# Kernel tuning notes

Measured on AMD Instinct MI355X. Metric: run time of the kernel, lower is better.

## Reference

```python
import jax, jax.numpy as jnp
import numpy as np

DIN = 256
N_RATIOS = 3          # cfg.ANCHOR_RATIOS = [0.5, 1, 2]
NC_SCORE = N_RATIOS * 2   # 6
NC_BBOX = N_RATIOS * 4    # 12
LEVEL_SHAPES = [(150, 250), (75, 125), (38, 63), (19, 32), (10, 16)]


def setup_inputs() -> dict:
    key = jax.random.key(0)
    ks = jax.random.split(key, 12)
    inp = {}
    for i, (h, w) in enumerate(LEVEL_SHAPES):
        inp[f"rpn_feat_p{i+2}"] = jax.random.normal(ks[i], (4, DIN, h, w), dtype=jnp.float32)
    inp["im_info"] = jnp.ones((4, 3), dtype=jnp.float32)
    s = 0.01
    inp["W_conv"] = jax.random.normal(ks[5], (512, DIN, 3, 3), dtype=jnp.float32) * s
    inp["b_conv"] = jnp.zeros((512,), dtype=jnp.float32)
    inp["W_cls"] = jax.random.normal(ks[6], (NC_SCORE, 512), dtype=jnp.float32) * s
    inp["b_cls"] = jnp.zeros((NC_SCORE,), dtype=jnp.float32)
    inp["W_box"] = jax.random.normal(ks[7], (NC_BBOX, 512), dtype=jnp.float32) * s
    inp["b_box"] = jnp.zeros((NC_BBOX,), dtype=jnp.float32)
    return inp


def _conv3x3(x, W, b):
    y = jax.lax.conv_general_dilated(
        x, W, window_strides=(1, 1), padding="SAME",
        dimension_numbers=("NCHW", "OIHW", "NCHW"))
    return y + b[None, :, None, None]


def _level_head(feat, W_conv, b_conv, W_cls, b_cls, W_box, b_box):
    B = feat.shape[0]
    conv1 = jax.nn.relu(_conv3x3(feat, W_conv, b_conv))            # [B,512,H,W]
    score = jnp.einsum("bchw,oc->bohw", conv1, W_cls) + b_cls[None, :, None, None]  # [B,6,H,W]
    bbox = jnp.einsum("bchw,oc->bohw", conv1, W_box) + b_box[None, :, None, None]   # [B,12,H,W]
    _, C, H, W = score.shape
    # reshape(x, 2): view(B, 2, C*H/2, W), softmax over dim 1, reshape back
    prob = jax.nn.softmax(score.reshape(B, 2, (C * H) // 2, W), axis=1).reshape(B, C, H, W)
    score_f = score.transpose(0, 2, 3, 1).reshape(B, -1, 2)
    prob_f = prob.transpose(0, 2, 3, 1).reshape(B, -1, 2)
    bbox_f = bbox.transpose(0, 2, 3, 1).reshape(B, -1, 4)
    return score_f, prob_f, bbox_f


def reference(rpn_feat_p2, rpn_feat_p3, rpn_feat_p4, rpn_feat_p5, rpn_feat_p6,
              im_info, W_conv, b_conv, W_cls, b_cls, W_box, b_box):
    feats = [rpn_feat_p2, rpn_feat_p3, rpn_feat_p4, rpn_feat_p5, rpn_feat_p6]
    scores, probs, boxes = [], [], []
    for f in feats:  # fixed 5 FPN levels
        s, p, b = _level_head(f, W_conv, b_conv, W_cls, b_cls, W_box, b_box)
        scores.append(s); probs.append(p); boxes.append(b)
    rpn_cls_score_alls = jnp.concatenate(scores, axis=1)            # [B, N, 2]
    rpn_cls_prob_alls = jnp.concatenate(probs, axis=1)              # [B, N, 2]
    rpn_bbox_pred_alls = jnp.concatenate(boxes, axis=1)             # [B, N, 4]
    return rpn_cls_score_alls, rpn_cls_prob_alls, rpn_bbox_pred_alls
```

## Files before the change

kernel.cpp:

```cpp
#include <hip/hip_runtime.h>
#include <stdint.h>


typedef __bf16 bf16x8 __attribute__((ext_vector_type(8)));
typedef float  f32x4  __attribute__((ext_vector_type(4)));

#define WS_WR2_OFF   0
#define WS_WH2_OFF   2359296
#define WS_SB_OFF    2392064
#define WS_FP_OFF    17100800
#define WS_TOTAL     123197440

__device__ __forceinline__ unsigned short f2bf(float f) {
    unsigned u = __builtin_bit_cast(unsigned, f);
    unsigned r = (u + 0x7FFF + ((u >> 16) & 1)) >> 16;
    return (unsigned short)r;
}

__device__ __forceinline__ void gl_lds16(const void* g, void* l) {
    __builtin_amdgcn_global_load_lds(
        (const __attribute__((address_space(1))) unsigned int*)g,
        (__attribute__((address_space(3))) unsigned int*)l, 16, 0, 0);
}

__global__ __launch_bounds__(256) void prep_weights(
    const float* __restrict__ Wc, const float* __restrict__ Wcls,
    const float* __restrict__ Wbox,
    unsigned short* __restrict__ wr2, unsigned short* __restrict__ wh2)
{
    int idx = blockIdx.x * 256 + threadIdx.x;
    if (idx < 1179648) {
        int o = idx / 2304;
        int k = idx - o * 2304;
        int r = k >> 8, c = k & 255;
        wr2[idx] = f2bf(Wc[o * 2304 + c * 9 + r]);
    } else {
        int i2 = idx - 1179648;
        if (i2 < 16384) {
            int j = i2 >> 9, o = i2 & 511;
            float v = (j < 6) ? Wcls[j * 512 + o]
                    : (j < 18) ? Wbox[(j - 6) * 512 + o] : 0.0f;
            wh2[j * 512 + o] = f2bf(v);
        }
    }
}

__global__ __launch_bounds__(256) void zero_rings(unsigned short* __restrict__ fpad)
{
    int idx = blockIdx.x * 256 + threadIdx.x;
    int b = idx / 50432;
    int rem = idx - b * 50432;
    int Wp, H, W; long lb;
    if (rem < 25728)      {               Wp=252; H=150; W=250; lb=32768    + (long)b*9805824; }
    else if (rem < 38656) { rem -= 25728; Wp=127; H=75;  W=125; lb=39288832 + (long)b*2503424; }
    else if (rem < 45248) { rem -= 38656; Wp=65;  H=38;  W=63;  lb=49335296 + (long)b*665600;  }
    else if (rem < 48640) { rem -= 45248; Wp=34;  H=19;  W=32;  lb=52030464 + (long)b*182784;  }
    else                  { rem -= 48640; Wp=18;  H=10;  W=16;  lb=52794368 + (long)b*55296;   }
    int c = rem >> 5, slot = rem & 31;
    int h, w;
    if (c < Wp)          { h = 0;     w = c; }
    else if (c < 2 * Wp) { h = H + 1; w = c - Wp; }
    else {
        int c2 = c - 2 * Wp;
        h = 1 + (c2 >> 1);
        w = (c2 & 1) ? (W + 1) : 0;
    }
    uint4 z = {0u, 0u, 0u, 0u};
    *(uint4*)(fpad + lb + (long)(h * Wp + w) * 256 + slot * 8) = z;
}

__global__ __launch_bounds__(256) void prep_feats(
    const float* __restrict__ f0, const float* __restrict__ f1,
    const float* __restrict__ f2, const float* __restrict__ f3,
    const float* __restrict__ f4, unsigned short* __restrict__ fpad)
{
    __shared__ unsigned short lds[64 * 258];
    int bi = blockIdx.x;
    int b = bi / 817;
    int r = bi - b * 817;
    const float* fsrc; int H, W, Wp, h, wb; long lb;
    if (r < 600)      { fsrc=f0; H=150; W=250; Wp=252; h=r>>2; wb=r&3; lb=32768    + (long)b*9805824; }
    else if (r < 750) { int rr=r-600; fsrc=f1; H=75; W=125; Wp=127; h=rr>>1; wb=rr&1; lb=39288832 + (long)b*2503424; }
    else if (r < 788) { fsrc=f2; H=38; W=63; Wp=65; h=r-750; wb=0; lb=49335296 + (long)b*665600; }
    else if (r < 807) { fsrc=f3; H=19; W=32; Wp=34; h=r-788; wb=0; lb=52030464 + (long)b*182784; }
    else              { fsrc=f4; H=10; W=16; Wp=18; h=r-807; wb=0; lb=52794368 + (long)b*55296; }
    const int t = threadIdx.x;
    const long cstr = (long)H * W;
    const int w = t & 63;
    const int wg = wb * 64 + w;
    const bool wv = (wg < W);
    const float* src = fsrc + (((long)b * 256) * H + h) * W + wg;
    unsigned* ldsw = (unsigned*)lds;
    #pragma unroll 4
    for (int it = 0; it < 32; ++it) {
        int c0 = (t >> 6) * 2 + it * 8;
        float v0 = wv ? src[(long)c0 * cstr] : 0.0f;
        float v1 = wv ? src[(long)(c0 + 1) * cstr] : 0.0f;
        unsigned pk = (unsigned)f2bf(v0) | ((unsigned)f2bf(v1) << 16);
        ldsw[w * 129 + (c0 >> 1)] = pk;
    }
    __syncthreads();
    #pragma unroll
    for (int k = 0; k < 8; ++k) {
        int g  = k * 256 + t;
        int px = g >> 5;
        int pg = wb * 64 + px;
        if (pg >= W) continue;
        int d0 = px * 129 + (g & 31) * 4;
        uint4 v;
        v.x = ldsw[d0]; v.y = ldsw[d0 + 1]; v.z = ldsw[d0 + 2]; v.w = ldsw[d0 + 3];
        unsigned short* dst = fpad + lb + (long)((h + 1) * Wp + (pg + 1)) * 256 + (g & 31) * 8;
        *(uint4*)dst = v;
    }
}

__global__ __launch_bounds__(256) void conv_main(
    const unsigned short* __restrict__ fpad,
    const unsigned short* __restrict__ wr2,
    const unsigned short* __restrict__ wh2,
    const float* __restrict__ b_conv,
    float* __restrict__ sbuf)
{
    __shared__ unsigned short smem[16384];
    const int tid = threadIdx.x;
    const int bid = blockIdx.x;
    const int tile = ((bid >> 5) << 3) + (bid & 7);
    const int chunk = (bid >> 3) & 3;
    if (tile >= 1596) return;
    int b = tile / 399;
    int tr = tile - b * 399;
    int Wp, lt; long lb;
    if (tr < 296)      { lt = tr;       Wp = 252; lb = 32768    + (long)b * 9805824; }
    else if (tr < 371) { lt = tr - 296; Wp = 127; lb = 39288832 + (long)b * 2503424; }
    else if (tr < 391) { lt = tr - 371; Wp = 65;  lb = 49335296 + (long)b * 665600;  }
    else if (tr < 397) { lt = tr - 391; Wp = 34;  lb = 52030464 + (long)b * 182784;  }
    else               { lt = tr - 397; Wp = 18;  lb = 52794368 + (long)b * 55296;   }

    const int arow  = tid >> 3;
    const int aslot = (tid & 7) ^ (arow & 7);
    const long apix = lb + (long)(Wp + lt * 128 + arow) * 256 + aslot * 8;
    const long bofs = (long)(chunk * 128 + arow) * 2304 + aslot * 8;

    const int wv = tid >> 6, lane = tid & 63;
    char* lA = (char*)smem + wv * 1024;
    char* lB = (char*)smem + 16384 + wv * 1024;
    const int mrow = (wv & 1) * 64, ncol = (wv >> 1) * 64;
    const int mr = lane & 15;
    const int kq = (lane >> 4) * 8;
    const int m7 = mr & 7;

    f32x4 acc[4][4];
    #pragma unroll
    for (int mt = 0; mt < 4; ++mt)
        #pragma unroll
        for (int nt = 0; nt < 4; ++nt) acc[mt][nt] = (f32x4){0.f, 0.f, 0.f, 0.f};

    for (int r = 0; r < 9; ++r) {
        const int doff = (r / 3 - 1) * Wp + (r % 3 - 1);
        const unsigned short* ga = fpad + apix + (long)doff * 256;
        const unsigned short* gb = wr2 + bofs + r * 256;
        for (int cb = 0; cb < 4; ++cb) {
            const unsigned short* ga2 = ga + cb * 64;
            const unsigned short* gb2 = gb + cb * 64;
            #pragma unroll
            for (int i = 0; i < 4; ++i) {
                gl_lds16(ga2 + i * 8192,  lA + i * 4096);
                gl_lds16(gb2 + i * 73728, lB + i * 4096);
            }
            __syncthreads();
            #pragma unroll
            for (int kk = 0; kk < 64; kk += 32) {
                const int sx = ((((kk >> 3) + (lane >> 4)) ^ m7) << 3);
                bf16x8 af[4], bfr[4];
                #pragma unroll
                for (int mt = 0; mt < 4; ++mt)
                    af[mt] = *(const bf16x8*)&smem[(mrow + mt * 16 + mr) * 64 + sx];
                #pragma unroll
                for (int nt = 0; nt < 4; ++nt)
                    bfr[nt] = *(const bf16x8*)&smem[8192 + (ncol + nt * 16 + mr) * 64 + sx];
                #pragma unroll
                for (int mt = 0; mt < 4; ++mt)
                    #pragma unroll
                    for (int nt = 0; nt < 4; ++nt)
                        acc[mt][nt] = __builtin_amdgcn_mfma_f32_16x16x32_bf16(
                            af[mt], bfr[nt], acc[mt][nt], 0, 0, 0);
            }
            __syncthreads();
        }
    }

    float bias[4];
    #pragma unroll
    for (int nt = 0; nt < 4; ++nt) bias[nt] = b_conv[chunk * 128 + ncol + nt * 16 + mr];
    #pragma unroll
    for (int mt = 0; mt < 4; ++mt)
        #pragma unroll
        for (int nt = 0; nt < 4; ++nt)
            #pragma unroll
            for (int q = 0; q < 4; ++q) {
                int row = mrow + mt * 16 + (lane >> 4) * 4 + q;
                int col = ncol + nt * 16 + mr;
                int sl  = (col >> 3) ^ (row & 7);
                smem[row * 128 + (sl << 3) + (col & 7)] =
                    f2bf(fmaxf(acc[mt][nt][q] + bias[nt], 0.0f));
            }
    __syncthreads();

    f32x4 acc2[2][2];
    #pragma unroll
    for (int mi = 0; mi < 2; ++mi)
        #pragma unroll
        for (int ni = 0; ni < 2; ++ni) acc2[mi][ni] = (f32x4){0.f, 0.f, 0.f, 0.f};
    #pragma unroll
    for (int ks = 0; ks < 4; ++ks) {
        const int sg = ks * 4 + (lane >> 4);
        bf16x8 ha[2], hb[2];
        #pragma unroll
        for (int mi = 0; mi < 2; ++mi) {
            int rowH = (wv * 2 + mi) * 16 + mr;
            ha[mi] = *(const bf16x8*)&smem[rowH * 128 + ((sg ^ m7) << 3)];
        }
        #pragma unroll
        for (int ni = 0; ni < 2; ++ni)
            hb[ni] = *(const bf16x8*)&wh2[(ni * 16 + mr) * 512 + chunk * 128 + ks * 32 + kq];
        #pragma unroll
        for (int mi = 0; mi < 2; ++mi)
            #pragma unroll
            for (int ni = 0; ni < 2; ++ni)
                acc2[mi][ni] = __builtin_amdgcn_mfma_f32_16x16x32_bf16(
                    ha[mi], hb[ni], acc2[mi][ni], 0, 0, 0);
    }
    const long slotbase = (long)tile * 128;
    #pragma unroll
    for (int ni = 0; ni < 2; ++ni) {
        int j = ni * 16 + mr;
        if (j < 18) {
            #pragma unroll
            for (int mi = 0; mi < 2; ++mi)
                #pragma unroll
                for (int q = 0; q < 4; ++q) {
                    int row = (wv * 2 + mi) * 16 + (lane >> 4) * 4 + q;
                    atomicAdd(&sbuf[(slotbase + row) * 18 + j], acc2[mi][ni][q]);
                }
        }
    }
}

__global__ __launch_bounds__(256) void finalize(
    const float* __restrict__ sbuf, const float* __restrict__ b_cls,
    const float* __restrict__ b_box, float* __restrict__ out)
{
    int idx = blockIdx.x * 256 + threadIdx.x;
    int tile = idx >> 7, m = idx & 127;
    int b = tile / 399;
    int tr = tile - b * 399;
    int hp, wp, H, W, noff;
    if (tr < 296)      { int f = 252 + (tr)       * 128 + m; hp = f / 252; wp = f - hp * 252; H = 150; W = 250; noff = 0; }
    else if (tr < 371) { int f = 127 + (tr - 296) * 128 + m; hp = f / 127; wp = f - hp * 127; H = 75;  W = 125; noff = 112500; }
    else if (tr < 391) { int f = 65  + (tr - 371) * 128 + m; hp = f / 65;  wp = f - hp * 65;  H = 38;  W = 63;  noff = 140625; }
    else if (tr < 397) { int f = 34  + (tr - 391) * 128 + m; hp = f / 34;  wp = f - hp * 34;  H = 19;  W = 32;  noff = 147807; }
    else               { int f = 18  + (tr - 397) * 128 + m; hp = f / 18;  wp = f - hp * 18;  H = 10;  W = 16;  noff = 149631; }
    if (hp < 1 || hp > H || wp < 1 || wp > W) return;

    const float* s = sbuf + (long)idx * 18;
    float sc[6], bb[12], pr[6];
    #pragma unroll
    for (int c = 0; c < 6; ++c) sc[c] = s[c] + b_cls[c];
    #pragma unroll
    for (int k = 0; k < 12; ++k) bb[k] = s[6 + k] + b_box[k];
    #pragma unroll
    for (int c = 0; c < 6; ++c) {
        int p = (c < 3) ? c + 3 : c - 3;
        pr[c] = 1.0f / (1.0f + expf(sc[p] - sc[c]));
    }
    int n = noff + ((hp - 1) * W + (wp - 1)) * 3;
    long o0 = ((long)b * 150111 + n) * 2;
    float* O0 = out + o0;
    float* O1 = out + 1200888 + o0;
    float* O2 = out + 2401776 + ((long)b * 150111 + n) * 4;
    #pragma unroll
    for (int c = 0; c < 6; ++c) { O0[c] = sc[c]; O1[c] = pr[c]; }
    #pragma unroll
    for (int k = 0; k < 12; ++k) O2[k] = bb[k];
}

extern "C" void kernel_launch(void* const* d_in, const int* in_sizes, int n_in,
                              void* d_out, int out_size, void* d_ws, size_t ws_size,
                              hipStream_t stream)
{
    const float* f0   = (const float*)d_in[0];
    const float* f1   = (const float*)d_in[1];
    const float* f2   = (const float*)d_in[2];
    const float* f3   = (const float*)d_in[3];
    const float* f4   = (const float*)d_in[4];
    const float* Wc   = (const float*)d_in[6];
    const float* bC   = (const float*)d_in[7];
    const float* Wcls = (const float*)d_in[8];
    const float* bcls = (const float*)d_in[9];
    const float* Wbox = (const float*)d_in[10];
    const float* bbox = (const float*)d_in[11];

    unsigned short* wr2  = (unsigned short*)((char*)d_ws + WS_WR2_OFF);
    unsigned short* wh2  = (unsigned short*)((char*)d_ws + WS_WH2_OFF);
    float*          sbuf = (float*)((char*)d_ws + WS_SB_OFF);
    unsigned short* fpad = (unsigned short*)((char*)d_ws + WS_FP_OFF);

    hipMemsetAsync((char*)d_ws + WS_SB_OFF, 0, (size_t)(WS_FP_OFF - WS_SB_OFF), stream);
    hipLaunchKernelGGL(prep_weights, dim3(4672), dim3(256), 0, stream, Wc, Wcls, Wbox, wr2, wh2);
    hipLaunchKernelGGL(zero_rings,   dim3(788),  dim3(256), 0, stream, fpad);
    hipLaunchKernelGGL(prep_feats,   dim3(3268), dim3(256), 0, stream, f0, f1, f2, f3, f4, fpad);
    hipLaunchKernelGGL(conv_main,    dim3(6400), dim3(256), 0, stream, fpad, wr2, wh2, bC, sbuf);
    hipLaunchKernelGGL(finalize,     dim3(798),  dim3(256), 0, stream, sbuf, bcls, bbox, (float*)d_out);
}
```

Measured before the change: 890.4 us.

## Enlarge conv GEMM tile to 256x256 with double-buffered LDS pipeline

Rewrites the implicit-GEMM conv kernel to use 512-thread blocks computing 256-pixel by 256-channel tiles instead of 128x128, with 128KB LDS double buffering. Loads for the next K step are issued asynchronously while the MFMAs for the current step run, using explicit waitcnt, barriers and setprio. The block index is swizzled for locality. This targets global/LDS traffic per FLOP and load latency stalls, at the cost of occupancy (one block per CU) and more complex synchronization.

```diff
diff --git a/kernel.cpp b/kernel.cpp
--- a/kernel.cpp
+++ b/kernel.cpp
@@ -114,94 +114,166 @@
     }
 }
 
-__global__ __launch_bounds__(256) void conv_main(
+__global__ __launch_bounds__(512) void conv_main(
     const unsigned short* __restrict__ fpad,
     const unsigned short* __restrict__ wr2,
     const unsigned short* __restrict__ wh2,
     const float* __restrict__ b_conv,
     float* __restrict__ sbuf)
 {
-    __shared__ unsigned short smem[16384];
+    __shared__ __align__(16) char smem[131072];
     const int tid = threadIdx.x;
     const int bid = blockIdx.x;
-    const int tile = ((bid >> 5) << 3) + (bid & 7);
-    const int chunk = (bid >> 3) & 3;
-    if (tile >= 1596) return;
-    int b = tile / 399;
-    int tr = tile - b * 399;
-    int Wp, lt; long lb;
-    if (tr < 296)      { lt = tr;       Wp = 252; lb = 32768    + (long)b * 9805824; }
-    else if (tr < 371) { lt = tr - 296; Wp = 127; lb = 39288832 + (long)b * 2503424; }
-    else if (tr < 391) { lt = tr - 371; Wp = 65;  lb = 49335296 + (long)b * 665600;  }
-    else if (tr < 397) { lt = tr - 391; Wp = 34;  lb = 52030464 + (long)b * 182784;  }
-    else               { lt = tr - 397; Wp = 18;  lb = 52794368 + (long)b * 55296;   }
-
-    const int arow  = tid >> 3;
-    const int aslot = (tid & 7) ^ (arow & 7);
-    const long apix = lb + (long)(Wp + lt * 128 + arow) * 256 + aslot * 8;
-    const long bofs = (long)(chunk * 128 + arow) * 2304 + aslot * 8;
+    const int swz = (bid & 7) * 200 + (bid >> 3);
+    const int tile = swz >> 1;
+    const int chunk = swz & 1;
+    const int b = tile / 200;
+    const int tr = tile - b * 200;
+    int Wp, lt, ot, rowlim = 256; long lb;
+    if (tr < 148)      { lt = tr;       Wp = 252; lb = 32768    + (long)b * 9805824; ot = b*399 + 2*lt; }
+    else if (tr < 186) { lt = tr - 148; Wp = 127; lb = 39288832 + (long)b * 2503424; ot = b*399 + 296 + 2*lt;
+                         if (lt == 37) rowlim = 128; }
+    else if (tr < 196) { lt = tr - 186; Wp = 65;  lb = 49335296 + (long)b * 665600;  ot = b*399 + 371 + 2*lt; }
+    else if (tr < 199) { lt = tr - 196; Wp = 34;  lb = 52030464 + (long)b * 182784;  ot = b*399 + 391 + 2*lt; }
+    else               { lt = 0;        Wp = 18;  lb = 52794368 + (long)b * 55296;   ot = b*399 + 397; }
 
     const int wv = tid >> 6, lane = tid & 63;
-    char* lA = (char*)smem + wv * 1024;
-    char* lB = (char*)smem + 16384 + wv * 1024;
-    const int mrow = (wv & 1) * 64, ncol = (wv >> 1) * 64;
-    const int mr = lane & 15;
-    const int kq = (lane >> 4) * 8;
+    const int srow  = lane >> 3;
+    const int gslot = (lane & 7) ^ srow;
+    const unsigned short* aBase = fpad + lb + (long)(Wp + lt*256 + wv*8 + srow) * 256 + gslot*8;
+    const unsigned short* bBase = wr2 + (long)(chunk*256 + wv*8 + srow) * 2304 + gslot*8;
+
+    const int wm = wv & 1, wn = wv >> 1;
+    const int mr = lane & 15, kq4 = lane >> 4;
     const int m7 = mr & 7;
-
-    f32x4 acc[4][4];
-    #pragma unroll
-    for (int mt = 0; mt < 4; ++mt)
+    const int aRd = wm * 16384 + mr * 128;
+    const int bRd = 32768 + (wn >> 1) * 16384 + ((wn & 1) * 64 + mr) * 128;
+    const int sw0 = ((kq4 ^ m7) << 4);
+    const int sw1 = (((4 + kq4) ^ m7) << 4);
+
+#define RD_A(bo_, mt_, sw_) (*(const bf16x8*)(smem + (bo_) + aRd + (mt_)*2048 + (sw_)))
+#define RD_B(bo_, nt_, sw_) (*(const bf16x8*)(smem + (bo_) + bRd + (nt_)*2048 + (sw_)))
+
+#define STAGE_A(bo_, kt_, h_) do {                                            \
+        const int r_ = (kt_) >> 2;                                            \
+        const int doff_ = (r_ / 3 - 1) * Wp + (r_ % 3 - 1);                   \
+        const unsigned short* g_ = aBase + ((long)((h_) * 128 + doff_)) * 256 \
+                                   + ((kt_) & 3) * 64;                        \
+        char* l_ = smem + (bo_) + (h_) * 16384 + wv * 1024;                   \
+        gl_lds16(g_,          l_);                                            \
+        gl_lds16(g_ + 16384,  l_ + 8192);                                     \
+    } while (0)
+
+#define STAGE_B(bo_, kt_, h_) do {                                            \
+        const unsigned short* g_ = bBase + (long)(h_) * 294912 + (kt_) * 64;  \
+        char* l_ = smem + (bo_) + 32768 + (h_) * 16384 + wv * 1024;           \
+        gl_lds16(g_,           l_);                                           \
+        gl_lds16(g_ + 147456,  l_ + 8192);                                    \
+    } while (0)
+
+#define MFMA16(d_, a_, b_) d_ = __builtin_amdgcn_mfma_f32_16x16x32_bf16(a_, b_, d_, 0, 0, 0)
+
+    f32x4 acc[8][4];
+    #pragma unroll
+    for (int mt = 0; mt < 8; ++mt)
         #pragma unroll
         for (int nt = 0; nt < 4; ++nt) acc[mt][nt] = (f32x4){0.f, 0.f, 0.f, 0.f};
 
-    for (int r = 0; r < 9; ++r) {
-        const int doff = (r / 3 - 1) * Wp + (r % 3 - 1);
-        const unsigned short* ga = fpad + apix + (long)doff * 256;
-        const unsigned short* gb = wr2 + bofs + r * 256;
-        for (int cb = 0; cb < 4; ++cb) {
-            const unsigned short* ga2 = ga + cb * 64;
-            const unsigned short* gb2 = gb + cb * 64;
-            #pragma unroll
-            for (int i = 0; i < 4; ++i) {
-                gl_lds16(ga2 + i * 8192,  lA + i * 4096);
-                gl_lds16(gb2 + i * 73728, lB + i * 4096);
-            }
-            __syncthreads();
-            #pragma unroll
-            for (int kk = 0; kk < 64; kk += 32) {
-                const int sx = ((((kk >> 3) + (lane >> 4)) ^ m7) << 3);
-                bf16x8 af[4], bfr[4];
-                #pragma unroll
-                for (int mt = 0; mt < 4; ++mt)
-                    af[mt] = *(const bf16x8*)&smem[(mrow + mt * 16 + mr) * 64 + sx];
-                #pragma unroll
-                for (int nt = 0; nt < 4; ++nt)
-                    bfr[nt] = *(const bf16x8*)&smem[8192 + (ncol + nt * 16 + mr) * 64 + sx];
-                #pragma unroll
-                for (int mt = 0; mt < 4; ++mt)
-                    #pragma unroll
-                    for (int nt = 0; nt < 4; ++nt)
-                        acc[mt][nt] = __builtin_amdgcn_mfma_f32_16x16x32_bf16(
-                            af[mt], bfr[nt], acc[mt][nt], 0, 0, 0);
-            }
-            __syncthreads();
-        }
+    STAGE_A(0, 0, 0); STAGE_A(0, 0, 1);
+    STAGE_B(0, 0, 0); STAGE_B(0, 0, 1);
+    STAGE_B(65536, 1, 0); STAGE_B(65536, 1, 1);
+    asm volatile("s_waitcnt vmcnt(4)" ::: "memory");
+    __builtin_amdgcn_s_barrier();
+
+    bf16x8 af[4][2], bfr[4][2];
+    #pragma unroll 2
+    for (int t = 0; t < 36; ++t) {
+        const int bo  = (t & 1) << 16;
+        const int bon = bo ^ 65536;
+
+        #pragma unroll
+        for (int mt = 0; mt < 4; ++mt) { af[mt][0] = RD_A(bo, mt, sw0); af[mt][1] = RD_A(bo, mt, sw1); }
+        #pragma unroll
+        for (int nt = 0; nt < 2; ++nt) { bfr[nt][0] = RD_B(bo, nt, sw0); bfr[nt][1] = RD_B(bo, nt, sw1); }
+        if (t < 35) STAGE_A(bon, t + 1, 0);
+        __builtin_amdgcn_s_barrier();
+        asm volatile("s_waitcnt lgkmcnt(0)" ::: "memory");
+        __builtin_amdgcn_sched_barrier(0);
+        __builtin_amdgcn_s_setprio(1);
+        #pragma unroll
+        for (int mt = 0; mt < 4; ++mt)
+            #pragma unroll
+            for (int nt = 0; nt < 2; ++nt) {
+                MFMA16(acc[mt][nt], af[mt][0], bfr[nt][0]);
+                MFMA16(acc[mt][nt], af[mt][1], bfr[nt][1]);
+            }
+        __builtin_amdgcn_s_setprio(0);
+        __builtin_amdgcn_s_barrier();
+
+        #pragma unroll
+        for (int nt = 2; nt < 4; ++nt) { bfr[nt][0] = RD_B(bo, nt, sw0); bfr[nt][1] = RD_B(bo, nt, sw1); }
+        if (t < 35) STAGE_A(bon, t + 1, 1);
+        __builtin_amdgcn_s_barrier();
+        asm volatile("s_waitcnt lgkmcnt(0)" ::: "memory");
+        __builtin_amdgcn_sched_barrier(0);
+        __builtin_amdgcn_s_setprio(1);
+        #pragma unroll
+        for (int mt = 0; mt < 4; ++mt)
+            #pragma unroll
+            for (int nt = 2; nt < 4; ++nt) {
+                MFMA16(acc[mt][nt], af[mt][0], bfr[nt][0]);
+                MFMA16(acc[mt][nt], af[mt][1], bfr[nt][1]);
+            }
+        __builtin_amdgcn_s_setprio(0);
+        __builtin_amdgcn_s_barrier();
+
+        #pragma unroll
+        for (int mt = 0; mt < 4; ++mt) { af[mt][0] = RD_A(bo, mt + 4, sw0); af[mt][1] = RD_A(bo, mt + 4, sw1); }
+        if (t < 34) STAGE_B(bo, t + 2, 0);
+        __builtin_amdgcn_s_barrier();
+        asm volatile("s_waitcnt lgkmcnt(0)" ::: "memory");
+        __builtin_amdgcn_sched_barrier(0);
+        __builtin_amdgcn_s_setprio(1);
+        #pragma unroll
+        for (int mt = 0; mt < 4; ++mt)
+            #pragma unroll
+            for (int nt = 0; nt < 2; ++nt) {
+                MFMA16(acc[mt + 4][nt], af[mt][0], bfr[nt][0]);
+                MFMA16(acc[mt + 4][nt], af[mt][1], bfr[nt][1]);
+            }
+        __builtin_amdgcn_s_setprio(0);
+        __builtin_amdgcn_s_barrier();
+
+        if (t < 34) STAGE_B(bo, t + 2, 1);
+        __builtin_amdgcn_s_barrier();
+        __builtin_amdgcn_s_setprio(1);
+        #pragma unroll
+        for (int mt = 0; mt < 4; ++mt)
+            #pragma unroll
+            for (int nt = 2; nt < 4; ++nt) {
+                MFMA16(acc[mt + 4][nt], af[mt][0], bfr[nt][0]);
+                MFMA16(acc[mt + 4][nt], af[mt][1], bfr[nt][1]);
+            }
+        __builtin_amdgcn_s_setprio(0);
+        if (t < 34) { asm volatile("s_waitcnt vmcnt(4)" ::: "memory"); }
+        else        { asm volatile("s_waitcnt vmcnt(0)" ::: "memory"); }
+        __builtin_amdgcn_s_barrier();
     }
 
     float bias[4];
-    #pragma unroll
-    for (int nt = 0; nt < 4; ++nt) bias[nt] = b_conv[chunk * 128 + ncol + nt * 16 + mr];
-    #pragma unroll
-    for (int mt = 0; mt < 4; ++mt)
+    const int ncol = wn * 64;
+    #pragma unroll
+    for (int nt = 0; nt < 4; ++nt) bias[nt] = b_conv[chunk * 256 + ncol + nt * 16 + mr];
+    #pragma unroll
+    for (int mt = 0; mt < 8; ++mt)
         #pragma unroll
         for (int nt = 0; nt < 4; ++nt)
             #pragma unroll
             for (int q = 0; q < 4; ++q) {
-                int row = mrow + mt * 16 + (lane >> 4) * 4 + q;
+                int row = wm * 128 + mt * 16 + kq4 * 4 + q;
                 int col = ncol + nt * 16 + mr;
                 int sl  = (col >> 3) ^ (row & 7);
-                smem[row * 128 + (sl << 3) + (col & 7)] =
+                *(unsigned short*)(smem + row * 512 + (sl << 4) + ((col & 7) << 1)) =
                     f2bf(fmaxf(acc[mt][nt][q] + bias[nt], 0.0f));
             }
     __syncthreads();
@@ -211,26 +283,18 @@
     for (int mi = 0; mi < 2; ++mi)
         #pragma unroll
         for (int ni = 0; ni < 2; ++ni) acc2[mi][ni] = (f32x4){0.f, 0.f, 0.f, 0.f};
-    #pragma unroll
-    for (int ks = 0; ks < 4; ++ks) {
-        const int sg = ks * 4 + (lane >> 4);
-        bf16x8 ha[2], hb[2];
-        #pragma unroll
-        for (int mi = 0; mi < 2; ++mi) {
-            int rowH = (wv * 2 + mi) * 16 + mr;
-            ha[mi] = *(const bf16x8*)&smem[rowH * 128 + ((sg ^ m7) << 3)];
-        }
-        #pragma unroll
-        for (int ni = 0; ni < 2; ++ni)
-            hb[ni] = *(const bf16x8*)&wh2[(ni * 16 + mr) * 512 + chunk * 128 + ks * 32 + kq];
-        #pragma unroll
-        for (int mi = 0; mi < 2; ++mi)
-            #pragma unroll
-            for (int ni = 0; ni < 2; ++ni)
-                acc2[mi][ni] = __builtin_amdgcn_mfma_f32_16x16x32_bf16(
-                    ha[mi], hb[ni], acc2[mi][ni], 0, 0, 0);
-    }
-    const long slotbase = (long)tile * 128;
+    const int hrow = wv * 32 + mr;
+    #pragma unroll
+    for (int ks = 0; ks < 8; ++ks) {
+        const int swh = (((ks * 4 + kq4) ^ m7) << 4);
+        bf16x8 ha0 = *(const bf16x8*)(smem + hrow * 512 + swh);
+        bf16x8 ha1 = *(const bf16x8*)(smem + (hrow + 16) * 512 + swh);
+        bf16x8 hb0 = *(const bf16x8*)&wh2[mr * 512 + chunk * 256 + ks * 32 + kq4 * 8];
+        bf16x8 hb1 = *(const bf16x8*)&wh2[(16 + mr) * 512 + chunk * 256 + ks * 32 + kq4 * 8];
+        MFMA16(acc2[0][0], ha0, hb0); MFMA16(acc2[0][1], ha0, hb1);
+        MFMA16(acc2[1][0], ha1, hb0); MFMA16(acc2[1][1], ha1, hb1);
+    }
+    const long slotbase = (long)ot * 128;
     #pragma unroll
     for (int ni = 0; ni < 2; ++ni) {
         int j = ni * 16 + mr;
@@ -239,11 +303,17 @@
             for (int mi = 0; mi < 2; ++mi)
                 #pragma unroll
                 for (int q = 0; q < 4; ++q) {
-                    int row = (wv * 2 + mi) * 16 + (lane >> 4) * 4 + q;
-                    atomicAdd(&sbuf[(slotbase + row) * 18 + j], acc2[mi][ni][q]);
+                    int row = wv * 32 + mi * 16 + kq4 * 4 + q;
+                    if (row < rowlim)
+                        atomicAdd(&sbuf[(slotbase + row) * 18 + j], acc2[mi][ni][q]);
                 }
         }
     }
+#undef RD_A
+#undef RD_B
+#undef STAGE_A
+#undef STAGE_B
+#undef MFMA16
 }
 
 __global__ __launch_bounds__(256) void finalize(
@@ -309,6 +379,6 @@
     hipLaunchKernelGGL(prep_weights, dim3(4672), dim3(256), 0, stream, Wc, Wcls, Wbox, wr2, wh2);
     hipLaunchKernelGGL(zero_rings,   dim3(788),  dim3(256), 0, stream, fpad);
     hipLaunchKernelGGL(prep_feats,   dim3(3268), dim3(256), 0, stream, f0, f1, f2, f3, f4, fpad);
-    hipLaunchKernelGGL(conv_main,    dim3(6400), dim3(256), 0, stream, fpad, wr2, wh2, bC, sbuf);
+    hipLaunchKernelGGL(conv_main,    dim3(1600), dim3(512), 0, stream, fpad, wr2, wh2, bC, sbuf);
     hipLaunchKernelGGL(finalize,     dim3(798),  dim3(256), 0, stream, sbuf, bcls, bbox, (float*)d_out);
 }
```

New measurement: 801.1 us. -10.0%, faster.
